# Optimization experiments

Measured on AMD Instinct MI355X. Metric: run time of the kernel, lower is better.

The kernel has to match this reference:

```python
import jax, jax.numpy as jnp
import numpy as np

B, T, C, H, D, E, K = 4, 1024, 1024, 16, 64, 8, 2
HID = 2 * D  # expert MLP hidden width (assumed 2*head_dim)
NEG = jnp.finfo(jnp.float32).min


def setup_inputs() -> dict:
    key = jax.random.key(0)
    ks = jax.random.split(key, 16)
    s = 0.02
    # rotary tables [max_pos, head_dim]
    inv_freq = 1.0 / (10000.0 ** (jnp.arange(0, D, 2, dtype=jnp.float32) / D))
    freqs = jnp.arange(T, dtype=jnp.float32)[:, None] * inv_freq[None, :]
    emb = jnp.concatenate([freqs, freqs], axis=-1)  # [T, D]
    return {
        "x": jax.random.normal(ks[0], (B, T, C), jnp.float32),
        "position_ids": jnp.sort(jax.random.randint(ks[1], (B, T), 0, T), axis=-1),
        "cos": jnp.cos(emb),
        "sin": jnp.sin(emb),
        "rq": s * jax.random.normal(ks[2], (D, E), jnp.float32),
        "rk": s * jax.random.normal(ks[3], (D, E), jnp.float32),
        "rv": s * jax.random.normal(ks[4], (D, E), jnp.float32),
        "q_w1": s * jax.random.normal(ks[5], (E, D, HID), jnp.float32),
        "q_w2": s * jax.random.normal(ks[6], (E, HID, D), jnp.float32),
        "k_w1": s * jax.random.normal(ks[7], (E, D, HID), jnp.float32),
        "k_w2": s * jax.random.normal(ks[8], (E, HID, D), jnp.float32),
        "v_w1": s * jax.random.normal(ks[9], (E, D, HID), jnp.float32),
        "v_w2": s * jax.random.normal(ks[10], (E, HID, D), jnp.float32),
        "o_w": s * jax.random.normal(ks[11], (C, C), jnp.float32),  # torch Linear weight [out,in]
    }


def _rotate_half(x):
    x1, x2 = x[..., : D // 2], x[..., D // 2:]
    return jnp.concatenate([-x2, x1], axis=-1)


def _moe_head_proj(xh, r_w, w1, w2):
    """Per-head top-k routed expert MLP. xh: [B,T,H,D]."""
    logits = jnp.einsum('bthd,de->bthe', xh, r_w)            # router logits
    vals, idx = jax.lax.top_k(logits, K)                     # [B,T,H,K]
    w = jax.nn.softmax(vals, axis=-1)
    onehot = jax.nn.one_hot(idx, E, dtype=xh.dtype)          # [B,T,H,K,E]
    w_full = jnp.einsum('bthk,bthke->bthe', w, onehot)       # scatter weights to all experts
    h = jax.nn.gelu(jnp.einsum('bthd,edf->bthef', xh, w1))   # all-expert hidden
    out = jnp.einsum('bthe,bthef,efg->bthg', w_full, h, w2)  # masked weighted combine
    return out, logits


def reference(x, position_ids, cos, sin, rq, rk, rv, q_w1, q_w2, k_w1, k_w2, v_w1, v_w2, o_w):
    xh = x.reshape(B, T, H, D)
    q, _ = _moe_head_proj(xh, rq, q_w1, q_w2)
    k, _ = _moe_head_proj(xh, rk, k_w1, k_w2)
    v, _ = _moe_head_proj(xh, rv, v_w1, v_w2)
    q = q.transpose(0, 2, 1, 3)  # [B,H,T,D]
    k = k.transpose(0, 2, 1, 3)
    v = v.transpose(0, 2, 1, 3)
    # RoPE
    c = cos[position_ids][:, None, :, :]  # [B,1,T,D]
    s = sin[position_ids][:, None, :, :]
    q = q * c + _rotate_half(q) * s
    k = k * c + _rotate_half(k) * s
    # causal SDPA
    scores = jnp.einsum('bhqd,bhkd->bhqk', q, k) / jnp.sqrt(jnp.float32(D))
    causal = jnp.tril(jnp.ones((T, T), dtype=bool))
    scores = jnp.where(causal, scores, NEG)
    attn = jax.nn.softmax(scores, axis=-1)
    out = jnp.einsum('bhqk,bhkd->bhqd', attn, v)
    out = out.transpose(0, 2, 1, 3).reshape(B, T, C)
    return out @ o_w.T
```

## Files before the change

### kernel.cpp

```cpp
#include <hip/hip_runtime.h>
#include <math.h>

#define BB 4
#define TT 1024
#define CCH 1024
#define HH 16
#define DD 64
#define EE 8
#define HID 128
#define CAP 8192
#define GEXP 504

typedef unsigned short u16;
typedef unsigned int u32;
typedef short bf16x8 __attribute__((ext_vector_type(8)));
typedef float f32x4 __attribute__((ext_vector_type(4)));

__device__ __forceinline__ u16 f2bf(float f) {
    unsigned int u = __float_as_uint(f);
    unsigned int r = (u + 0x7FFFu + ((u >> 16) & 1u)) >> 16;
    return (u16)r;
}
__device__ __forceinline__ u16 f2bf_f(float f) {
    return (u16)((__float_as_uint(f) + 0x8000u) >> 16);
}
__device__ __forceinline__ u32 pkbf(float lo, float hi) {
    u32 a = __float_as_uint(lo) + 0x8000u;
    u32 b = __float_as_uint(hi) + 0x8000u;
    return __builtin_amdgcn_perm(b, a, 0x07060302u);
}
__device__ __forceinline__ float gelu_fast(float z) {
    float t = z * z;
    float wn = __builtin_fmaf(t, -0.07135481283f, -1.5957691216f);
    float e = __expf(z * wn);
    return __fdividef(z, 1.f + e);
}

#define GLD16(gp, lp) __builtin_amdgcn_global_load_lds( \
    (const __attribute__((address_space(1))) u32*)(gp), \
    (__attribute__((address_space(3))) u32*)(lp), 16, 0, 0)

__global__ __launch_bounds__(256) void router_kernel(
    const float* __restrict__ x,
    const float* __restrict__ rq, const float* __restrict__ rk, const float* __restrict__ rv,
    unsigned int* __restrict__ counts,
    unsigned int* __restrict__ idxbuf, float2* __restrict__ wtbuf)
{
    const int tid = threadIdx.x;
    const unsigned int g = blockIdx.x * 256 + tid;

    __shared__ float rS[3][64][8];
    __shared__ int lcnt[192];
    __shared__ int lbase[192];

    for (int i = tid; i < 1536; i += 256) {
        int p = i >> 9, rem = i & 511;
        const float* rp = (p == 0) ? rq : (p == 1) ? rk : rv;
        rS[p][rem >> 3][rem & 7] = rp[rem];
    }
    if (tid < 192) lcnt[tid] = 0;
    __syncthreads();

    float lg[3][8];
    #pragma unroll
    for (int p = 0; p < 3; ++p)
        #pragma unroll
        for (int e = 0; e < 8; ++e) lg[p][e] = 0.f;

    const float* xr = x + (size_t)g * 64;
    for (int i4 = 0; i4 < 16; ++i4) {
        float4 xv = ((const float4*)xr)[i4];
        float xa[4] = {xv.x, xv.y, xv.z, xv.w};
        #pragma unroll
        for (int m = 0; m < 4; ++m) {
            int d = i4 * 4 + m;
            #pragma unroll
            for (int p = 0; p < 3; ++p) {
                float4 r0 = *(const float4*)&rS[p][d][0];
                float4 r1 = *(const float4*)&rS[p][d][4];
                lg[p][0] += xa[m] * r0.x; lg[p][1] += xa[m] * r0.y;
                lg[p][2] += xa[m] * r0.z; lg[p][3] += xa[m] * r0.w;
                lg[p][4] += xa[m] * r1.x; lg[p][5] += xa[m] * r1.y;
                lg[p][6] += xa[m] * r1.z; lg[p][7] += xa[m] * r1.w;
            }
        }
    }

    int ppe[3]; float2 pw[3]; int slot[3];
    #pragma unroll
    for (int p = 0; p < 3; ++p) {
        int i1 = 0; float v1 = lg[p][0];
        #pragma unroll
        for (int e = 1; e < 8; ++e) { if (lg[p][e] > v1) { v1 = lg[p][e]; i1 = e; } }
        int i2 = -1; float v2 = -3.402823466e38f;
        #pragma unroll
        for (int e = 0; e < 8; ++e) { if (e != i1 && lg[p][e] > v2) { v2 = lg[p][e]; i2 = e; } }
        float z = __expf(v2 - v1);
        float inv = 1.f / (1.f + z);
        float wa = inv, wb = z * inv;
        int lo = min(i1, i2), hi = max(i1, i2);
        float wlo = (i1 < i2) ? wa : wb;
        float whi = (i1 < i2) ? wb : wa;
        int pel = p * 64 + lo * 8 + hi;
        ppe[p] = pel; pw[p] = make_float2(wlo, whi);
        slot[p] = atomicAdd(&lcnt[pel], 1);
    }
    __syncthreads();
    if (tid < 192) {
        int c = lcnt[tid];
        lbase[tid] = c ? (int)atomicAdd(&counts[tid], (unsigned int)c) : 0;
    }
    __syncthreads();
    #pragma unroll
    for (int p = 0; p < 3; ++p) {
        int pos = lbase[ppe[p]] + slot[p];
        if (pos < CAP) {
            idxbuf[ppe[p] * CAP + pos] = g;
            wtbuf[ppe[p] * CAP + pos]  = pw[p];
        }
    }
}

__global__ __launch_bounds__(128) void sched_kernel(
    const unsigned int* __restrict__ counts, unsigned int* __restrict__ blockinfo)
{
    const int tid = threadIdx.x;
    __shared__ int nsub[84];
    __shared__ int extra[84];
    __shared__ int frac[84];
    __shared__ int alloc[84];
    __shared__ int startS[84];
    __shared__ int nnzS, totalS, rem2S;

    if (tid < 84) {
        int p = tid / 28, q = tid - 28 * p, lo = 0;
        while (q >= 7 - lo) { q -= 7 - lo; ++lo; }
        int hi = lo + 1 + q;
        int n = (int)counts[p * 64 + lo * 8 + hi];
        if (n > CAP) n = CAP;
        nsub[tid] = (n + 31) >> 5;
    }
    __syncthreads();
    if (tid == 0) {
        int tot = 0, nz = 0;
        for (int i = 0; i < 84; ++i) { tot += nsub[i]; nz += (nsub[i] > 0); }
        totalS = tot; nnzS = nz;
    }
    __syncthreads();
    const int R = GEXP - nnzS;
    if (tid < 84) {
        if (nsub[tid] > 0) {
            int e = (int)(((long long)nsub[tid] * R) / totalS);
            extra[tid] = e;
            frac[tid] = nsub[tid] * R - e * totalS;
        } else { extra[tid] = 0; frac[tid] = -1; }
    }
    __syncthreads();
    if (tid == 0) {
        int se = 0;
        for (int i = 0; i < 84; ++i) se += extra[i];
        rem2S = GEXP - nnzS - se;
    }
    __syncthreads();
    if (tid < 84) {
        if (nsub[tid] > 0) {
            int rank = 0;
            for (int j = 0; j < 84; ++j)
                if (nsub[j] > 0 && (frac[j] > frac[tid] || (frac[j] == frac[tid] && j < tid))) ++rank;
            alloc[tid] = 1 + extra[tid] + (rank < rem2S ? 1 : 0);
        } else alloc[tid] = 0;
    }
    __syncthreads();
    if (tid == 0) {
        int s = 0;
        for (int i = 0; i < 84; ++i) { startS[i] = s; s += alloc[i]; }
    }
    __syncthreads();
    if (tid < 84) {
        int a = alloc[tid], st = startS[tid];
        for (int c = 0; c < a; ++c)
            blockinfo[st + c] = (unsigned)tid | ((unsigned)c << 8) | ((unsigned)a << 20);
    }
}

__global__ __launch_bounds__(256) void wcvt_kernel(
    const float* __restrict__ qw1, const float* __restrict__ kw1, const float* __restrict__ vw1,
    const float* __restrict__ qw2, const float* __restrict__ kw2, const float* __restrict__ vw2,
    u16* __restrict__ img1, u16* __restrict__ img2)
{
    int t = blockIdx.x * 256 + threadIdx.x;
    u16 tmp[8];
    if (t < 24576) {
        int c = t & 7, f = (t >> 3) & 127, e = (t >> 10) & 7, p = t >> 13;
        const float* w1 = ((p == 0) ? qw1 : (p == 1) ? kw1 : vw1) + e * 8192;
        int dbase = 8 * (c ^ (f & 7));
        #pragma unroll
        for (int j = 0; j < 8; ++j) tmp[j] = f2bf(w1[(dbase + j) * 128 + f]);
        uint4 ov;
        ov.x = (u32)tmp[0] | ((u32)tmp[1] << 16);
        ov.y = (u32)tmp[2] | ((u32)tmp[3] << 16);
        ov.z = (u32)tmp[4] | ((u32)tmp[5] << 16);
        ov.w = (u32)tmp[6] | ((u32)tmp[7] << 16);
        ((uint4*)img1)[t] = ov;
    } else {
        int i = t - 24576;
        int c = i & 15, g = (i >> 4) & 63, e = (i >> 10) & 7, p = i >> 13;
        const float* w2 = ((p == 0) ? qw2 : (p == 1) ? kw2 : vw2) + e * 8192;
        int fbase = 8 * (c ^ (g & 15));
        #pragma unroll
        for (int j = 0; j < 8; ++j) tmp[j] = f2bf(w2[(fbase + j) * 64 + g]);
        uint4 ov;
        ov.x = (u32)tmp[0] | ((u32)tmp[1] << 16);
        ov.y = (u32)tmp[2] | ((u32)tmp[3] << 16);
        ov.z = (u32)tmp[4] | ((u32)tmp[5] << 16);
        ov.w = (u32)tmp[6] | ((u32)tmp[7] << 16);
        ((uint4*)img2)[i] = ov;
    }
}

__global__ __launch_bounds__(512, 2) void expert_kernel(
    const float* __restrict__ x, const int* __restrict__ pos_ids,
    const float* __restrict__ cosb, const float* __restrict__ sinb,
    const u16* __restrict__ img1, const u16* __restrict__ img2,
    const unsigned int* __restrict__ counts,
    const unsigned int* __restrict__ idxbuf, const float2* __restrict__ wtbuf,
    const unsigned int* __restrict__ blockinfo,
    u16* __restrict__ qb, u16* __restrict__ kb, u16* __restrict__ vb)
{
    const int tid = threadIdx.x;
    const unsigned int info = blockinfo[blockIdx.x];
    const int pe84 = info & 255;
    const int chunk = (info >> 8) & 0xFFF;
    const int nch = info >> 20;
    const int p = pe84 / 28;
    int q28 = pe84 - p * 28;
    int lo = 0;
    while (q28 >= 7 - lo) { q28 -= 7 - lo; ++lo; }
    const int hi = lo + 1 + q28;
    const int pe = p * 64 + lo * 8 + hi;

    int n = (int)counts[pe]; if (n == 0) return; if (n > CAP) n = CAP;

    u16* outp = (p == 0) ? qb : (p == 1) ? kb : vb;
    const unsigned int* il = idxbuf + pe * CAP;
    const float2* wl = wtbuf + pe * CAP;

    __shared__ __align__(16) u16 wsh[32768];

    {
        const u16* a0 = img1 + (p * 8 + lo) * 8192;
        const u16* b0 = img2 + (p * 8 + lo) * 8192;
        const u16* a1 = img1 + (p * 8 + hi) * 8192;
        const u16* b1 = img2 + (p * 8 + hi) * 8192;
        #pragma unroll
        for (int k = 0; k < 2; ++k) {
            int o = (k * 512 + tid) * 8;
            GLD16(a0 + o, wsh + o);
            GLD16(b0 + o, wsh + 8192 + o);
            GLD16(a1 + o, wsh + 16384 + o);
            GLD16(b1 + o, wsh + 24576 + o);
        }
    }
    __syncthreads();

    const int lane = tid & 63, w = tid >> 6, quad = lane >> 4, m16 = lane & 15;
    const int f7 = m16 & 7;
    const int sA = m16 + ((quad & 1) << 5);
    const int sB = sA + 16;
    const int wid = chunk * 8 + w;
    const int WRK = nch * 8;
    const int nsub = (n + 31) >> 5;

    for (int s = wid; s < nsub; s += WRK) {
        const int base = s * 32;
        unsigned int gtok = 0, obase = 0; float wlo_ = 0.f, whi_ = 0.f;
        int posv = 0, valid = 0;
        if (lane < 32) {
            int j = base + lane;
            valid = (j < n);
            int jc = valid ? j : (n - 1);
            gtok = il[jc];
            float2 wv = wl[jc];
            wlo_ = valid ? wv.x : 0.f; whi_ = valid ? wv.y : 0.f;
            unsigned int b_ = gtok >> 14, h_ = gtok & 15, t_ = (gtok >> 4) & 1023;
            obase = ((b_ * 16 + h_) * 1024 + t_) * 64;
            posv = pos_ids[b_ * 1024 + t_];
        }

        float wf00 = __shfl(wlo_, m16, 64);
        float wf10 = __shfl(whi_, m16, 64);
        float wf01 = __shfl(wlo_, 16 + m16, 64);
        float wf11 = __shfl(whi_, 16 + m16, 64);

        bf16x8 Afr[2][2];
        #pragma unroll
        for (int mt2 = 0; mt2 < 2; ++mt2) {
            unsigned int gm = (unsigned int)__shfl((int)gtok, mt2 * 16 + m16, 64);
            const float* xr = x + (size_t)gm * 64 + 8 * quad;
            float4 xa0 = *(const float4*)(xr);
            float4 xa1 = *(const float4*)(xr + 4);
            float4 xb0 = *(const float4*)(xr + 32);
            float4 xb1 = *(const float4*)(xr + 36);
            bf16x8 A0, A1;
            A0[0] = (short)f2bf_f(xa0.x); A0[1] = (short)f2bf_f(xa0.y);
            A0[2] = (short)f2bf_f(xa0.z); A0[3] = (short)f2bf_f(xa0.w);
            A0[4] = (short)f2bf_f(xa1.x); A0[5] = (short)f2bf_f(xa1.y);
            A0[6] = (short)f2bf_f(xa1.z); A0[7] = (short)f2bf_f(xa1.w);
            A1[0] = (short)f2bf_f(xb0.x); A1[1] = (short)f2bf_f(xb0.y);
            A1[2] = (short)f2bf_f(xb0.z); A1[3] = (short)f2bf_f(xb0.w);
            A1[4] = (short)f2bf_f(xb1.x); A1[5] = (short)f2bf_f(xb1.y);
            A1[6] = (short)f2bf_f(xb1.z); A1[7] = (short)f2bf_f(xb1.w);
            Afr[mt2][0] = A0; Afr[mt2][1] = A1;
        }

        f32x4 acc2[2][4];
        #pragma unroll
        for (int mt2 = 0; mt2 < 2; ++mt2)
            #pragma unroll
            for (int nt = 0; nt < 4; ++nt) acc2[mt2][nt] = (f32x4){0.f, 0.f, 0.f, 0.f};

        #pragma unroll 1
        for (int ekk = 0; ekk < 8; ++ekk) {
            const int e = ekk >> 2;
            const int kk = ekk & 3;
            const u16* w1b = wsh + e * 16384;
            const u16* w2b = w1b + 8192;
            const float wt0 = e ? wf10 : wf00;
            const float wt1 = e ? wf11 : wf01;

            f32x4 c[2][2];
            #pragma unroll
            for (int ntl = 0; ntl < 2; ++ntl) {
                const int f = 16 * (2 * kk + ntl) + m16;
                const u16* w1f = w1b + f * 64;
                bf16x8 wa = *(const bf16x8*)(w1f + (((quad    ) ^ f7) << 3));
                bf16x8 wb = *(const bf16x8*)(w1f + (((quad + 4) ^ f7) << 3));
                #pragma unroll
                for (int mt2 = 0; mt2 < 2; ++mt2) {
                    f32x4 t = (f32x4){0.f, 0.f, 0.f, 0.f};
                    t = __builtin_amdgcn_mfma_f32_16x16x32_bf16(wa, Afr[mt2][0], t, 0, 0, 0);
                    c[ntl][mt2] = __builtin_amdgcn_mfma_f32_16x16x32_bf16(wb, Afr[mt2][1], t, 0, 0, 0);
                }
            }
            const int c2base = (((4 * kk + quad) ^ m16) << 3);
            #pragma unroll
            for (int mt2 = 0; mt2 < 2; ++mt2) {
                const float wt = mt2 ? wt1 : wt0;
                u32 pl0, ph0, pl1, ph1;
                {
                    float g0 = wt * gelu_fast(c[0][mt2][0]);
                    float g1 = wt * gelu_fast(c[0][mt2][1]);
                    float g2 = wt * gelu_fast(c[0][mt2][2]);
                    float g3 = wt * gelu_fast(c[0][mt2][3]);
                    pl0 = pkbf(g0, g1); ph0 = pkbf(g2, g3);
                    g0 = wt * gelu_fast(c[1][mt2][0]);
                    g1 = wt * gelu_fast(c[1][mt2][1]);
                    g2 = wt * gelu_fast(c[1][mt2][2]);
                    g3 = wt * gelu_fast(c[1][mt2][3]);
                    pl1 = pkbf(g0, g1); ph1 = pkbf(g2, g3);
                }
                u32 q0l = (u32)__shfl((int)pl0, sA, 64);
                u32 q1l = (u32)__shfl((int)pl1, sA, 64);
                u32 q0h = (u32)__shfl((int)ph0, sA, 64);
                u32 q1h = (u32)__shfl((int)ph1, sA, 64);
                u32 r0l = (u32)__shfl((int)pl0, sB, 64);
                u32 r1l = (u32)__shfl((int)pl1, sB, 64);
                u32 r0h = (u32)__shfl((int)ph0, sB, 64);
                u32 r1h = (u32)__shfl((int)ph1, sB, 64);
                const bool hisel = (quad & 2);
                union { u32 u[4]; bf16x8 v; } a2;
                a2.u[0] = hisel ? q1l : q0l;
                a2.u[1] = hisel ? q1h : q0h;
                a2.u[2] = hisel ? r1l : r0l;
                a2.u[3] = hisel ? r1h : r0h;
                #pragma unroll
                for (int nt2 = 0; nt2 < 4; ++nt2) {
                    const u16* w2f = w2b + (16 * nt2 + m16) * 128 + c2base;
                    bf16x8 b2 = *(const bf16x8*)w2f;
                    acc2[mt2][nt2] = __builtin_amdgcn_mfma_f32_16x16x32_bf16(a2.v, b2, acc2[mt2][nt2], 0, 0, 0);
                }
            }
        }

        #pragma unroll
        for (int mt2 = 0; mt2 < 2; ++mt2) {
            #pragma unroll
            for (int r = 0; r < 4; ++r) {
                int tk = mt2 * 16 + 4 * quad + r;
                int   pos_r = __shfl(posv, tk, 64);
                unsigned int ob = (unsigned int)__shfl((int)obase, tk, 64);
                int   val_r = __shfl(valid, tk, 64);
                if (p < 2) {
                    #pragma unroll
                    for (int ntp = 0; ntp < 2; ++ntp) {
                        int d = 16 * ntp + m16;
                        float v1 = acc2[mt2][ntp][r];
                        float v2 = acc2[mt2][ntp + 2][r];
                        float cd = cosb[pos_r * 64 + d];
                        float sd = sinb[pos_r * 64 + d];
                        if (val_r) {
                            outp[ob + d]      = f2bf(v1 * cd - v2 * sd);
                            outp[ob + d + 32] = f2bf(v2 * cd + v1 * sd);
                        }
                    }
                } else {
                    #pragma unroll
                    for (int nt = 0; nt < 4; ++nt) {
                        float v = acc2[mt2][nt][r];
                        if (val_r) outp[ob + 16 * nt + m16] = f2bf(v);
                    }
                }
            }
        }
    }
}

__global__ __launch_bounds__(256) void cvt_bf16_kernel(
    const float* __restrict__ in, u16* __restrict__ out, int n4)
{
    int i = blockIdx.x * 256 + threadIdx.x;
    if (i >= n4) return;
    float4 v = ((const float4*)in)[i];
    unsigned int lov = (unsigned int)f2bf(v.x) | ((unsigned int)f2bf(v.y) << 16);
    unsigned int hiv = (unsigned int)f2bf(v.z) | ((unsigned int)f2bf(v.w) << 16);
    ((uint2*)out)[i] = make_uint2(lov, hiv);
}

__global__ __launch_bounds__(256) void attn_kernel(
    const u16* __restrict__ qbp, const u16* __restrict__ kbp,
    const u16* __restrict__ vbp, u16* __restrict__ ao)
{
    const int tid = threadIdx.x;
    const int i8 = blockIdx.x & 7;
    const int plane_i = blockIdx.x >> 3;
    const int h = plane_i & 15, b = plane_i >> 4;
    const size_t plane = (size_t)plane_i * 1024 * 64;
    const u16* qp = qbp + plane;
    const u16* kp = kbp + plane;
    const u16* vp = vbp + plane;

    const int w = tid >> 6, lane = tid & 63, quad = lane >> 4, m16 = lane & 15;
    const int row = tid >> 2, seg = tid & 3;
    const int kjv = tid & 63, dgv = tid >> 6;

    __shared__ u16 Ks[64][72];
    __shared__ u16 Vt[64][72];
    __shared__ u16 Ps[4][16][72];

    #pragma unroll 1
    for (int half = 0; half < 2; ++half) {
        const int qt = half ? (15 - i8) : i8;
        const int q0 = qt * 64;

        const u16* qrow = &qp[(size_t)(q0 + 16 * w + m16) * 64 + 8 * quad];
        bf16x8 aq0 = *(const bf16x8*)(qrow);
        bf16x8 aq1 = *(const bf16x8*)(qrow + 32);

        uint4 kr0, kr1; ushort4 vr0, vr1, vr2, vr3;
        {
            const uint4* src = (const uint4*)&kp[(size_t)row * 64 + seg * 16];
            kr0 = src[0]; kr1 = src[1];
            const u16* vb2 = &vp[(size_t)kjv * 64 + dgv * 4];
            vr0 = *(const ushort4*)(vb2);
            vr1 = *(const ushort4*)(vb2 + 16);
            vr2 = *(const ushort4*)(vb2 + 32);
            vr3 = *(const ushort4*)(vb2 + 48);
        }

        float m_r[4], l_r[4];
        #pragma unroll
        for (int i = 0; i < 4; ++i) { m_r[i] = -1e30f; l_r[i] = 0.f; }
        f32x4 oacc[4];
        #pragma unroll
        for (int i = 0; i < 4; ++i) oacc[i] = (f32x4){0.f, 0.f, 0.f, 0.f};

        for (int kt = 0; kt <= qt; ++kt) {
            __syncthreads();
            {
                uint4* dst = (uint4*)&Ks[row][seg * 16];
                dst[0] = kr0; dst[1] = kr1;
                int d0 = dgv * 4;
                Vt[d0 + 0][kjv] = vr0.x; Vt[d0 + 1][kjv] = vr0.y;
                Vt[d0 + 2][kjv] = vr0.z; Vt[d0 + 3][kjv] = vr0.w;
                Vt[d0 + 16][kjv] = vr1.x; Vt[d0 + 17][kjv] = vr1.y;
                Vt[d0 + 18][kjv] = vr1.z; Vt[d0 + 19][kjv] = vr1.w;
                Vt[d0 + 32][kjv] = vr2.x; Vt[d0 + 33][kjv] = vr2.y;
                Vt[d0 + 34][kjv] = vr2.z; Vt[d0 + 35][kjv] = vr2.w;
                Vt[d0 + 48][kjv] = vr3.x; Vt[d0 + 49][kjv] = vr3.y;
                Vt[d0 + 50][kjv] = vr3.z; Vt[d0 + 51][kjv] = vr3.w;
            }
            __syncthreads();
            if (kt < qt) {
                const int k0n = (kt + 1) * 64;
                const uint4* src = (const uint4*)&kp[(size_t)(k0n + row) * 64 + seg * 16];
                kr0 = src[0]; kr1 = src[1];
                const u16* vb2 = &vp[(size_t)(k0n + kjv) * 64 + dgv * 4];
                vr0 = *(const ushort4*)(vb2);
                vr1 = *(const ushort4*)(vb2 + 16);
                vr2 = *(const ushort4*)(vb2 + 32);
                vr3 = *(const ushort4*)(vb2 + 48);
            }

            f32x4 sv[4];
            #pragma unroll
            for (int ct = 0; ct < 4; ++ct) {
                bf16x8 bk0 = *(const bf16x8*)&Ks[16 * ct + m16][8 * quad];
                bf16x8 bk1 = *(const bf16x8*)&Ks[16 * ct + m16][32 + 8 * quad];
                f32x4 acc = (f32x4){0.f, 0.f, 0.f, 0.f};
                acc = __builtin_amdgcn_mfma_f32_16x16x32_bf16(aq0, bk0, acc, 0, 0, 0);
                acc = __builtin_amdgcn_mfma_f32_16x16x32_bf16(aq1, bk1, acc, 0, 0, 0);
                sv[ct] = acc;
            }

            float s[4][4];
            const bool diag = (kt == qt);
            #pragma unroll
            for (int ct = 0; ct < 4; ++ct)
                #pragma unroll
                for (int reg = 0; reg < 4; ++reg) {
                    float v = sv[ct][reg] * 0.125f;
                    if (diag) {
                        int col = 16 * ct + m16;
                        int rw = 16 * w + 4 * quad + reg;
                        if (col > rw) v = -1e30f;
                    }
                    s[ct][reg] = v;
                }

            float nm[4], al[4];
            #pragma unroll
            for (int reg = 0; reg < 4; ++reg) {
                float rm = fmaxf(fmaxf(s[0][reg], s[1][reg]), fmaxf(s[2][reg], s[3][reg]));
                #pragma unroll
                for (int off = 1; off < 16; off <<= 1) rm = fmaxf(rm, __shfl_xor(rm, off, 16));
                float mn = fmaxf(m_r[reg], rm);
                nm[reg] = mn;
                al[reg] = __expf(m_r[reg] - mn);
            }
            #pragma unroll
            for (int reg = 0; reg < 4; ++reg) {
                float sum = 0.f;
                #pragma unroll
                for (int ct = 0; ct < 4; ++ct) {
                    float pv = __expf(s[ct][reg] - nm[reg]);
                    s[ct][reg] = pv;
                    sum += pv;
                }
                #pragma unroll
                for (int off = 1; off < 16; off <<= 1) sum += __shfl_xor(sum, off, 16);
                l_r[reg] = l_r[reg] * al[reg] + sum;
                m_r[reg] = nm[reg];
            }

            #pragma unroll
            for (int ct = 0; ct < 4; ++ct)
                #pragma unroll
                for (int reg = 0; reg < 4; ++reg)
                    Ps[w][4 * quad + reg][16 * ct + m16] = f2bf(s[ct][reg]);

            #pragma unroll
            for (int dt = 0; dt < 4; ++dt)
                #pragma unroll
                for (int reg = 0; reg < 4; ++reg) oacc[dt][reg] *= al[reg];

            bf16x8 ap0 = *(const bf16x8*)&Ps[w][m16][8 * quad];
            bf16x8 ap1 = *(const bf16x8*)&Ps[w][m16][32 + 8 * quad];
            #pragma unroll
            for (int dt = 0; dt < 4; ++dt) {
                bf16x8 bv0 = *(const bf16x8*)&Vt[16 * dt + m16][8 * quad];
                bf16x8 bv1 = *(const bf16x8*)&Vt[16 * dt + m16][32 + 8 * quad];
                oacc[dt] = __builtin_amdgcn_mfma_f32_16x16x32_bf16(ap0, bv0, oacc[dt], 0, 0, 0);
                oacc[dt] = __builtin_amdgcn_mfma_f32_16x16x32_bf16(ap1, bv1, oacc[dt], 0, 0, 0);
            }
        }

        #pragma unroll
        for (int reg = 0; reg < 4; ++reg) {
            float linv = 1.f / l_r[reg];
            int rw = q0 + 16 * w + 4 * quad + reg;
            size_t base = ((size_t)(b * 1024) + rw) * 1024 + h * 64;
            #pragma unroll
            for (int dt = 0; dt < 4; ++dt)
                ao[base + 16 * dt + m16] = f2bf(oacc[dt][reg] * linv);
        }
    }
}

__global__ __launch_bounds__(256) void oproj_kernel(
    const u16* __restrict__ A, const u16* __restrict__ Bw,
    float* __restrict__ out)
{
    const int tid = threadIdx.x;
    const int bn = blockIdx.x & 7;
    const int bm = blockIdx.x >> 3;
    const int m0 = bm * 128, n0 = bn * 128;
    const int w = tid >> 6, lane = tid & 63, quad = lane >> 4, m16 = lane & 15;
    const int wm = (w >> 1) * 64, wn = (w & 1) * 64;

    __shared__ u16 As[128][32];
    __shared__ u16 Bs[128][32];

    f32x4 acc[4][4];
    #pragma unroll
    for (int mt = 0; mt < 4; ++mt)
        #pragma unroll
        for (int nt = 0; nt < 4; ++nt) acc[mt][nt] = (f32x4){0.f, 0.f, 0.f, 0.f};

    for (int k0 = 0; k0 < 1024; k0 += 32) {
        __syncthreads();
        {
            int rw = tid >> 1, sg = (tid & 1) * 16;
            const uint4* srcA = (const uint4*)&A[(size_t)(m0 + rw) * 1024 + k0 + sg];
            uint4 a0 = srcA[0], a1 = srcA[1];
            uint4* dstA = (uint4*)&As[rw][sg];
            dstA[0] = a0; dstA[1] = a1;
            const uint4* srcB = (const uint4*)&Bw[(size_t)(n0 + rw) * 1024 + k0 + sg];
            uint4 b0 = srcB[0], b1 = srcB[1];
            uint4* dstB = (uint4*)&Bs[rw][sg];
            dstB[0] = b0; dstB[1] = b1;
        }
        __syncthreads();
        bf16x8 af[4], bf_[4];
        #pragma unroll
        for (int mt = 0; mt < 4; ++mt) af[mt] = *(const bf16x8*)&As[wm + 16 * mt + m16][8 * quad];
        #pragma unroll
        for (int nt = 0; nt < 4; ++nt) bf_[nt] = *(const bf16x8*)&Bs[wn + 16 * nt + m16][8 * quad];
        #pragma unroll
        for (int mt = 0; mt < 4; ++mt)
            #pragma unroll
            for (int nt = 0; nt < 4; ++nt)
                acc[mt][nt] = __builtin_amdgcn_mfma_f32_16x16x32_bf16(af[mt], bf_[nt], acc[mt][nt], 0, 0, 0);
    }
    #pragma unroll
    for (int mt = 0; mt < 4; ++mt)
        #pragma unroll
        for (int nt = 0; nt < 4; ++nt)
            #pragma unroll
            for (int reg = 0; reg < 4; ++reg)
                out[(size_t)(m0 + wm + 16 * mt + 4 * quad + reg) * 1024 + n0 + wn + 16 * nt + m16] =
                    acc[mt][nt][reg];
}

extern "C" void kernel_launch(void* const* d_in, const int* in_sizes, int n_in,
                              void* d_out, int out_size, void* d_ws, size_t ws_size,
                              hipStream_t stream) {
    (void)in_sizes; (void)n_in; (void)out_size; (void)ws_size;
    const float* x    = (const float*)d_in[0];
    const int*   pid  = (const int*)  d_in[1];
    const float* cosb = (const float*)d_in[2];
    const float* sinb = (const float*)d_in[3];
    const float* rq   = (const float*)d_in[4];
    const float* rk   = (const float*)d_in[5];
    const float* rv   = (const float*)d_in[6];
    const float* qw1  = (const float*)d_in[7];
    const float* qw2  = (const float*)d_in[8];
    const float* kw1  = (const float*)d_in[9];
    const float* kw2  = (const float*)d_in[10];
    const float* vw1  = (const float*)d_in[11];
    const float* vw2  = (const float*)d_in[12];
    const float* ow   = (const float*)d_in[13];
    float* out = (float*)d_out;

    const size_t MB = 1u << 20;
    char* wsb = (char*)d_ws;
    u16* qb   = (u16*)(wsb + 0 * MB);
    u16* kb   = (u16*)(wsb + 8 * MB);
    u16* vb   = (u16*)(wsb + 16 * MB);
    u16* aobf = (u16*)(wsb + 24 * MB);
    u16* owbf = (u16*)(wsb + 32 * MB);
    unsigned int* idxbuf = (unsigned int*)(wsb + 34 * MB);
    float2*       wtbuf  = (float2*)(wsb + 41 * MB);
    unsigned int* counts = (unsigned int*)(wsb + 54 * MB);
    unsigned int* blockinfo = (unsigned int*)(wsb + 54 * MB + 4096);
    u16* w1img = (u16*)(wsb + 56 * MB);
    u16* w2img = (u16*)(wsb + 57 * MB);

    hipMemsetAsync(counts, 0, 1024, stream);

    hipLaunchKernelGGL(wcvt_kernel, dim3(192), dim3(256), 0, stream,
                       qw1, kw1, vw1, qw2, kw2, vw2, w1img, w2img);
    hipLaunchKernelGGL(router_kernel, dim3(256), dim3(256), 0, stream,
                       x, rq, rk, rv, counts, idxbuf, wtbuf);
    hipLaunchKernelGGL(sched_kernel, dim3(1), dim3(128), 0, stream,
                       counts, blockinfo);
    hipLaunchKernelGGL(cvt_bf16_kernel, dim3(1024), dim3(256), 0, stream,
                       ow, owbf, 1024 * 1024 / 4);
    hipLaunchKernelGGL(expert_kernel, dim3(GEXP), dim3(512), 0, stream,
                       x, pid, cosb, sinb, w1img, w2img,
                       counts, idxbuf, wtbuf, blockinfo, qb, kb, vb);
    hipLaunchKernelGGL(attn_kernel, dim3(512), dim3(256), 0, stream,
                       qb, kb, vb, aobf);
    hipLaunchKernelGGL(oproj_kernel, dim3(256), dim3(256), 0, stream,
                       aobf, owbf, out);
}
```

Measured before the change: 247.6 us.

## Fuse weight conversion, router and o_w cast into one prep kernel; split attention tiles

After: 282.5 us. 1.14x slower.

```diff
diff --git a/kernel.cpp b/kernel.cpp
--- a/kernel.cpp
+++ b/kernel.cpp
@@ -40,83 +40,132 @@
     (const __attribute__((address_space(1))) u32*)(gp), \
     (__attribute__((address_space(3))) u32*)(lp), 16, 0, 0)
 
-__global__ __launch_bounds__(256) void router_kernel(
+__global__ __launch_bounds__(256) void prep_kernel(
     const float* __restrict__ x,
     const float* __restrict__ rq, const float* __restrict__ rk, const float* __restrict__ rv,
     unsigned int* __restrict__ counts,
-    unsigned int* __restrict__ idxbuf, float2* __restrict__ wtbuf)
+    unsigned int* __restrict__ idxbuf, float2* __restrict__ wtbuf,
+    const float* __restrict__ qw1, const float* __restrict__ kw1, const float* __restrict__ vw1,
+    const float* __restrict__ qw2, const float* __restrict__ kw2, const float* __restrict__ vw2,
+    u16* __restrict__ img1, u16* __restrict__ img2,
+    const float* __restrict__ ow, u16* __restrict__ owbf)
 {
+    const int bi = blockIdx.x;
     const int tid = threadIdx.x;
-    const unsigned int g = blockIdx.x * 256 + tid;
-
-    __shared__ float rS[3][64][8];
-    __shared__ int lcnt[192];
-    __shared__ int lbase[192];
-
-    for (int i = tid; i < 1536; i += 256) {
-        int p = i >> 9, rem = i & 511;
-        const float* rp = (p == 0) ? rq : (p == 1) ? rk : rv;
-        rS[p][rem >> 3][rem & 7] = rp[rem];
-    }
-    if (tid < 192) lcnt[tid] = 0;
-    __syncthreads();
-
-    float lg[3][8];
-    #pragma unroll
-    for (int p = 0; p < 3; ++p)
-        #pragma unroll
-        for (int e = 0; e < 8; ++e) lg[p][e] = 0.f;
-
-    const float* xr = x + (size_t)g * 64;
-    for (int i4 = 0; i4 < 16; ++i4) {
-        float4 xv = ((const float4*)xr)[i4];
-        float xa[4] = {xv.x, xv.y, xv.z, xv.w};
-        #pragma unroll
-        for (int m = 0; m < 4; ++m) {
-            int d = i4 * 4 + m;
-            #pragma unroll
-            for (int p = 0; p < 3; ++p) {
-                float4 r0 = *(const float4*)&rS[p][d][0];
-                float4 r1 = *(const float4*)&rS[p][d][4];
-                lg[p][0] += xa[m] * r0.x; lg[p][1] += xa[m] * r0.y;
-                lg[p][2] += xa[m] * r0.z; lg[p][3] += xa[m] * r0.w;
-                lg[p][4] += xa[m] * r1.x; lg[p][5] += xa[m] * r1.y;
-                lg[p][6] += xa[m] * r1.z; lg[p][7] += xa[m] * r1.w;
+
+    if (bi < 192) {
+        int t = bi * 256 + tid;
+        u16 tmp[8];
+        if (t < 24576) {
+            int c = t & 7, f = (t >> 3) & 127, e = (t >> 10) & 7, p = t >> 13;
+            const float* w1 = ((p == 0) ? qw1 : (p == 1) ? kw1 : vw1) + e * 8192;
+            int dbase = 8 * (c ^ (f & 7));
+            #pragma unroll
+            for (int j = 0; j < 8; ++j) tmp[j] = f2bf(w1[(dbase + j) * 128 + f]);
+            uint4 ov;
+            ov.x = (u32)tmp[0] | ((u32)tmp[1] << 16);
+            ov.y = (u32)tmp[2] | ((u32)tmp[3] << 16);
+            ov.z = (u32)tmp[4] | ((u32)tmp[5] << 16);
+            ov.w = (u32)tmp[6] | ((u32)tmp[7] << 16);
+            ((uint4*)img1)[t] = ov;
+        } else {
+            int i = t - 24576;
+            int c = i & 15, g = (i >> 4) & 63, e = (i >> 10) & 7, p = i >> 13;
+            const float* w2 = ((p == 0) ? qw2 : (p == 1) ? kw2 : vw2) + e * 8192;
+            int fbase = 8 * (c ^ (g & 15));
+            #pragma unroll
+            for (int j = 0; j < 8; ++j) tmp[j] = f2bf(w2[(fbase + j) * 64 + g]);
+            uint4 ov;
+            ov.x = (u32)tmp[0] | ((u32)tmp[1] << 16);
+            ov.y = (u32)tmp[2] | ((u32)tmp[3] << 16);
+            ov.z = (u32)tmp[4] | ((u32)tmp[5] << 16);
+            ov.w = (u32)tmp[6] | ((u32)tmp[7] << 16);
+            ((uint4*)img2)[i] = ov;
+        }
+        return;
+    }
+
+    if (bi < 1216) {
+        int i = (bi - 192) * 256 + tid;
+        float4 v = ((const float4*)ow)[i];
+        unsigned int lov = (unsigned int)f2bf(v.x) | ((unsigned int)f2bf(v.y) << 16);
+        unsigned int hiv = (unsigned int)f2bf(v.z) | ((unsigned int)f2bf(v.w) << 16);
+        ((uint2*)owbf)[i] = make_uint2(lov, hiv);
+        return;
+    }
+
+    {
+        const unsigned int g = (bi - 1216) * 256 + tid;
+
+        __shared__ float rS[3][64][8];
+        __shared__ int lcnt[192];
+        __shared__ int lbase[192];
+
+        for (int i = tid; i < 1536; i += 256) {
+            int p = i >> 9, rem = i & 511;
+            const float* rp = (p == 0) ? rq : (p == 1) ? rk : rv;
+            rS[p][rem >> 3][rem & 7] = rp[rem];
+        }
+        if (tid < 192) lcnt[tid] = 0;
+        __syncthreads();
+
+        float lg[3][8];
+        #pragma unroll
+        for (int p = 0; p < 3; ++p)
+            #pragma unroll
+            for (int e = 0; e < 8; ++e) lg[p][e] = 0.f;
+
+        const float* xr = x + (size_t)g * 64;
+        for (int i4 = 0; i4 < 16; ++i4) {
+            float4 xv = ((const float4*)xr)[i4];
+            float xa[4] = {xv.x, xv.y, xv.z, xv.w};
+            #pragma unroll
+            for (int m = 0; m < 4; ++m) {
+                int d = i4 * 4 + m;
+                #pragma unroll
+                for (int p = 0; p < 3; ++p) {
+                    float4 r0 = *(const float4*)&rS[p][d][0];
+                    float4 r1 = *(const float4*)&rS[p][d][4];
+                    lg[p][0] += xa[m] * r0.x; lg[p][1] += xa[m] * r0.y;
+                    lg[p][2] += xa[m] * r0.z; lg[p][3] += xa[m] * r0.w;
+                    lg[p][4] += xa[m] * r1.x; lg[p][5] += xa[m] * r1.y;
+                    lg[p][6] += xa[m] * r1.z; lg[p][7] += xa[m] * r1.w;
+                }
             }
         }
-    }
-
-    int ppe[3]; float2 pw[3]; int slot[3];
-    #pragma unroll
-    for (int p = 0; p < 3; ++p) {
-        int i1 = 0; float v1 = lg[p][0];
-        #pragma unroll
-        for (int e = 1; e < 8; ++e) { if (lg[p][e] > v1) { v1 = lg[p][e]; i1 = e; } }
-        int i2 = -1; float v2 = -3.402823466e38f;
-        #pragma unroll
-        for (int e = 0; e < 8; ++e) { if (e != i1 && lg[p][e] > v2) { v2 = lg[p][e]; i2 = e; } }
-        float z = __expf(v2 - v1);
-        float inv = 1.f / (1.f + z);
-        float wa = inv, wb = z * inv;
-        int lo = min(i1, i2), hi = max(i1, i2);
-        float wlo = (i1 < i2) ? wa : wb;
-        float whi = (i1 < i2) ? wb : wa;
-        int pel = p * 64 + lo * 8 + hi;
-        ppe[p] = pel; pw[p] = make_float2(wlo, whi);
-        slot[p] = atomicAdd(&lcnt[pel], 1);
-    }
-    __syncthreads();
-    if (tid < 192) {
-        int c = lcnt[tid];
-        lbase[tid] = c ? (int)atomicAdd(&counts[tid], (unsigned int)c) : 0;
-    }
-    __syncthreads();
-    #pragma unroll
-    for (int p = 0; p < 3; ++p) {
-        int pos = lbase[ppe[p]] + slot[p];
-        if (pos < CAP) {
-            idxbuf[ppe[p] * CAP + pos] = g;
-            wtbuf[ppe[p] * CAP + pos]  = pw[p];
+
+        int ppe[3]; float2 pw[3]; int slot[3];
+        #pragma unroll
+        for (int p = 0; p < 3; ++p) {
+            int i1 = 0; float v1 = lg[p][0];
+            #pragma unroll
+            for (int e = 1; e < 8; ++e) { if (lg[p][e] > v1) { v1 = lg[p][e]; i1 = e; } }
+            int i2 = -1; float v2 = -3.402823466e38f;
+            #pragma unroll
+            for (int e = 0; e < 8; ++e) { if (e != i1 && lg[p][e] > v2) { v2 = lg[p][e]; i2 = e; } }
+            float z = __expf(v2 - v1);
+            float inv = 1.f / (1.f + z);
+            float wa = inv, wb = z * inv;
+            int lo = min(i1, i2), hi = max(i1, i2);
+            float wlo = (i1 < i2) ? wa : wb;
+            float whi = (i1 < i2) ? wb : wa;
+            int pel = p * 64 + lo * 8 + hi;
+            ppe[p] = pel; pw[p] = make_float2(wlo, whi);
+            slot[p] = atomicAdd(&lcnt[pel], 1);
+        }
+        __syncthreads();
+        if (tid < 192) {
+            int c = lcnt[tid];
+            lbase[tid] = c ? (int)atomicAdd(&counts[tid], (unsigned int)c) : 0;
+        }
+        __syncthreads();
+        #pragma unroll
+        for (int p = 0; p < 3; ++p) {
+            int pos = lbase[ppe[p]] + slot[p];
+            if (pos < CAP) {
+                idxbuf[ppe[p] * CAP + pos] = g;
+                wtbuf[ppe[p] * CAP + pos]  = pw[p];
+            }
         }
     }
 }
@@ -180,41 +229,6 @@
         int a = alloc[tid], st = startS[tid];
         for (int c = 0; c < a; ++c)
             blockinfo[st + c] = (unsigned)tid | ((unsigned)c << 8) | ((unsigned)a << 20);
-    }
-}
-
-__global__ __launch_bounds__(256) void wcvt_kernel(
-    const float* __restrict__ qw1, const float* __restrict__ kw1, const float* __restrict__ vw1,
-    const float* __restrict__ qw2, const float* __restrict__ kw2, const float* __restrict__ vw2,
-    u16* __restrict__ img1, u16* __restrict__ img2)
-{
-    int t = blockIdx.x * 256 + threadIdx.x;
-    u16 tmp[8];
-    if (t < 24576) {
-        int c = t & 7, f = (t >> 3) & 127, e = (t >> 10) & 7, p = t >> 13;
-        const float* w1 = ((p == 0) ? qw1 : (p == 1) ? kw1 : vw1) + e * 8192;
-        int dbase = 8 * (c ^ (f & 7));
-        #pragma unroll
-        for (int j = 0; j < 8; ++j) tmp[j] = f2bf(w1[(dbase + j) * 128 + f]);
-        uint4 ov;
-        ov.x = (u32)tmp[0] | ((u32)tmp[1] << 16);
-        ov.y = (u32)tmp[2] | ((u32)tmp[3] << 16);
-        ov.z = (u32)tmp[4] | ((u32)tmp[5] << 16);
-        ov.w = (u32)tmp[6] | ((u32)tmp[7] << 16);
-        ((uint4*)img1)[t] = ov;
-    } else {
-        int i = t - 24576;
-        int c = i & 15, g = (i >> 4) & 63, e = (i >> 10) & 7, p = i >> 13;
-        const float* w2 = ((p == 0) ? qw2 : (p == 1) ? kw2 : vw2) + e * 8192;
-        int fbase = 8 * (c ^ (g & 15));
-        #pragma unroll
-        for (int j = 0; j < 8; ++j) tmp[j] = f2bf(w2[(fbase + j) * 64 + g]);
-        uint4 ov;
-        ov.x = (u32)tmp[0] | ((u32)tmp[1] << 16);
-        ov.y = (u32)tmp[2] | ((u32)tmp[3] << 16);
-        ov.z = (u32)tmp[4] | ((u32)tmp[5] << 16);
-        ov.w = (u32)tmp[6] | ((u32)tmp[7] << 16);
-        ((uint4*)img2)[i] = ov;
     }
 }
 
@@ -415,24 +429,13 @@
     }
 }
 
-__global__ __launch_bounds__(256) void cvt_bf16_kernel(
-    const float* __restrict__ in, u16* __restrict__ out, int n4)
-{
-    int i = blockIdx.x * 256 + threadIdx.x;
-    if (i >= n4) return;
-    float4 v = ((const float4*)in)[i];
-    unsigned int lov = (unsigned int)f2bf(v.x) | ((unsigned int)f2bf(v.y) << 16);
-    unsigned int hiv = (unsigned int)f2bf(v.z) | ((unsigned int)f2bf(v.w) << 16);
-    ((uint2*)out)[i] = make_uint2(lov, hiv);
-}
-
 __global__ __launch_bounds__(256) void attn_kernel(
     const u16* __restrict__ qbp, const u16* __restrict__ kbp,
     const u16* __restrict__ vbp, u16* __restrict__ ao)
 {
     const int tid = threadIdx.x;
-    const int i8 = blockIdx.x & 7;
-    const int plane_i = blockIdx.x >> 3;
+    const int qt = 15 - (blockIdx.x & 15);
+    const int plane_i = blockIdx.x >> 4;
     const int h = plane_i & 15, b = plane_i >> 4;
     const size_t plane = (size_t)plane_i * 1024 * 64;
     const u16* qp = qbp + plane;
@@ -447,142 +450,138 @@
     __shared__ u16 Vt[64][72];
     __shared__ u16 Ps[4][16][72];
 
-    #pragma unroll 1
-    for (int half = 0; half < 2; ++half) {
-        const int qt = half ? (15 - i8) : i8;
-        const int q0 = qt * 64;
-
-        const u16* qrow = &qp[(size_t)(q0 + 16 * w + m16) * 64 + 8 * quad];
-        bf16x8 aq0 = *(const bf16x8*)(qrow);
-        bf16x8 aq1 = *(const bf16x8*)(qrow + 32);
-
-        uint4 kr0, kr1; ushort4 vr0, vr1, vr2, vr3;
+    const int q0 = qt * 64;
+
+    const u16* qrow = &qp[(size_t)(q0 + 16 * w + m16) * 64 + 8 * quad];
+    bf16x8 aq0 = *(const bf16x8*)(qrow);
+    bf16x8 aq1 = *(const bf16x8*)(qrow + 32);
+
+    uint4 kr0, kr1; ushort4 vr0, vr1, vr2, vr3;
+    {
+        const uint4* src = (const uint4*)&kp[(size_t)row * 64 + seg * 16];
+        kr0 = src[0]; kr1 = src[1];
+        const u16* vb2 = &vp[(size_t)kjv * 64 + dgv * 4];
+        vr0 = *(const ushort4*)(vb2);
+        vr1 = *(const ushort4*)(vb2 + 16);
+        vr2 = *(const ushort4*)(vb2 + 32);
+        vr3 = *(const ushort4*)(vb2 + 48);
+    }
+
+    float m_r[4], l_r[4];
+    #pragma unroll
+    for (int i = 0; i < 4; ++i) { m_r[i] = -1e30f; l_r[i] = 0.f; }
+    f32x4 oacc[4];
+    #pragma unroll
+    for (int i = 0; i < 4; ++i) oacc[i] = (f32x4){0.f, 0.f, 0.f, 0.f};
+
+    for (int kt = 0; kt <= qt; ++kt) {
+        __syncthreads();
         {
-            const uint4* src = (const uint4*)&kp[(size_t)row * 64 + seg * 16];
+            uint4* dst = (uint4*)&Ks[row][seg * 16];
+            dst[0] = kr0; dst[1] = kr1;
+            int d0 = dgv * 4;
+            Vt[d0 + 0][kjv] = vr0.x; Vt[d0 + 1][kjv] = vr0.y;
+            Vt[d0 + 2][kjv] = vr0.z; Vt[d0 + 3][kjv] = vr0.w;
+            Vt[d0 + 16][kjv] = vr1.x; Vt[d0 + 17][kjv] = vr1.y;
+            Vt[d0 + 18][kjv] = vr1.z; Vt[d0 + 19][kjv] = vr1.w;
+            Vt[d0 + 32][kjv] = vr2.x; Vt[d0 + 33][kjv] = vr2.y;
+            Vt[d0 + 34][kjv] = vr2.z; Vt[d0 + 35][kjv] = vr2.w;
+            Vt[d0 + 48][kjv] = vr3.x; Vt[d0 + 49][kjv] = vr3.y;
+            Vt[d0 + 50][kjv] = vr3.z; Vt[d0 + 51][kjv] = vr3.w;
+        }
+        __syncthreads();
+        if (kt < qt) {
+            const int k0n = (kt + 1) * 64;
+            const uint4* src = (const uint4*)&kp[(size_t)(k0n + row) * 64 + seg * 16];
             kr0 = src[0]; kr1 = src[1];
-            const u16* vb2 = &vp[(size_t)kjv * 64 + dgv * 4];
+            const u16* vb2 = &vp[(size_t)(k0n + kjv) * 64 + dgv * 4];
             vr0 = *(const ushort4*)(vb2);
             vr1 = *(const ushort4*)(vb2 + 16);
             vr2 = *(const ushort4*)(vb2 + 32);
             vr3 = *(const ushort4*)(vb2 + 48);
         }
 
-        float m_r[4], l_r[4];
-        #pragma unroll
-        for (int i = 0; i < 4; ++i) { m_r[i] = -1e30f; l_r[i] = 0.f; }
-        f32x4 oacc[4];
-        #pragma unroll
-        for (int i = 0; i < 4; ++i) oacc[i] = (f32x4){0.f, 0.f, 0.f, 0.f};
-
-        for (int kt = 0; kt <= qt; ++kt) {
-            __syncthreads();
-            {
-                uint4* dst = (uint4*)&Ks[row][seg * 16];
-                dst[0] = kr0; dst[1] = kr1;
-                int d0 = dgv * 4;
-                Vt[d0 + 0][kjv] = vr0.x; Vt[d0 + 1][kjv] = vr0.y;
-                Vt[d0 + 2][kjv] = vr0.z; Vt[d0 + 3][kjv] = vr0.w;
-                Vt[d0 + 16][kjv] = vr1.x; Vt[d0 + 17][kjv] = vr1.y;
-                Vt[d0 + 18][kjv] = vr1.z; Vt[d0 + 19][kjv] = vr1.w;
-                Vt[d0 + 32][kjv] = vr2.x; Vt[d0 + 33][kjv] = vr2.y;
-                Vt[d0 + 34][kjv] = vr2.z; Vt[d0 + 35][kjv] = vr2.w;
-                Vt[d0 + 48][kjv] = vr3.x; Vt[d0 + 49][kjv] = vr3.y;
-                Vt[d0 + 50][kjv] = vr3.z; Vt[d0 + 51][kjv] = vr3.w;
+        f32x4 sv[4];
+        #pragma unroll
+        for (int ct = 0; ct < 4; ++ct) {
+            bf16x8 bk0 = *(const bf16x8*)&Ks[16 * ct + m16][8 * quad];
+            bf16x8 bk1 = *(const bf16x8*)&Ks[16 * ct + m16][32 + 8 * quad];
+            f32x4 acc = (f32x4){0.f, 0.f, 0.f, 0.f};
+            acc = __builtin_amdgcn_mfma_f32_16x16x32_bf16(aq0, bk0, acc, 0, 0, 0);
+            acc = __builtin_amdgcn_mfma_f32_16x16x32_bf16(aq1, bk1, acc, 0, 0, 0);
+            sv[ct] = acc;
+        }
+
+        float s[4][4];
+        const bool diag = (kt == qt);
+        #pragma unroll
+        for (int ct = 0; ct < 4; ++ct)
+            #pragma unroll
+            for (int reg = 0; reg < 4; ++reg) {
+                float v = sv[ct][reg] * 0.125f;
+                if (diag) {
+                    int col = 16 * ct + m16;
+                    int rw = 16 * w + 4 * quad + reg;
+                    if (col > rw) v = -1e30f;
+                }
+                s[ct][reg] = v;
             }
-            __syncthreads();
-            if (kt < qt) {
-                const int k0n = (kt + 1) * 64;
-                const uint4* src = (const uint4*)&kp[(size_t)(k0n + row) * 64 + seg * 16];
-                kr0 = src[0]; kr1 = src[1];
-                const u16* vb2 = &vp[(size_t)(k0n + kjv) * 64 + dgv * 4];
-                vr0 = *(const ushort4*)(vb2);
-                vr1 = *(const ushort4*)(vb2 + 16);
-                vr2 = *(const ushort4*)(vb2 + 32);
-                vr3 = *(const ushort4*)(vb2 + 48);
+
+        float nm[4], al[4];
+        #pragma unroll
+        for (int reg = 0; reg < 4; ++reg) {
+            float rm = fmaxf(fmaxf(s[0][reg], s[1][reg]), fmaxf(s[2][reg], s[3][reg]));
+            #pragma unroll
+            for (int off = 1; off < 16; off <<= 1) rm = fmaxf(rm, __shfl_xor(rm, off, 16));
+            float mn = fmaxf(m_r[reg], rm);
+            nm[reg] = mn;
+            al[reg] = __expf(m_r[reg] - mn);
+        }
+        #pragma unroll
+        for (int reg = 0; reg < 4; ++reg) {
+            float sum = 0.f;
+            #pragma unroll
+            for (int ct = 0; ct < 4; ++ct) {
+                float pv = __expf(s[ct][reg] - nm[reg]);
+                s[ct][reg] = pv;
+                sum += pv;
             }
-
-            f32x4 sv[4];
-            #pragma unroll
-            for (int ct = 0; ct < 4; ++ct) {
-                bf16x8 bk0 = *(const bf16x8*)&Ks[16 * ct + m16][8 * quad];
-                bf16x8 bk1 = *(const bf16x8*)&Ks[16 * ct + m16][32 + 8 * quad];
-                f32x4 acc = (f32x4){0.f, 0.f, 0.f, 0.f};
-                acc = __builtin_amdgcn_mfma_f32_16x16x32_bf16(aq0, bk0, acc, 0, 0, 0);
-                acc = __builtin_amdgcn_mfma_f32_16x16x32_bf16(aq1, bk1, acc, 0, 0, 0);
-                sv[ct] = acc;
-            }
-
-            float s[4][4];
-            const bool diag = (kt == qt);
-            #pragma unroll
-            for (int ct = 0; ct < 4; ++ct)
-                #pragma unroll
-                for (int reg = 0; reg < 4; ++reg) {
-                    float v = sv[ct][reg] * 0.125f;
-                    if (diag) {
-                        int col = 16 * ct + m16;
-                        int rw = 16 * w + 4 * quad + reg;
-                        if (col > rw) v = -1e30f;
-                    }
-                    s[ct][reg] = v;
-                }
-
-            float nm[4], al[4];
-            #pragma unroll
-            for (int reg = 0; reg < 4; ++reg) {
-                float rm = fmaxf(fmaxf(s[0][reg], s[1][reg]), fmaxf(s[2][reg], s[3][reg]));
-                #pragma unroll
-                for (int off = 1; off < 16; off <<= 1) rm = fmaxf(rm, __shfl_xor(rm, off, 16));
-                float mn = fmaxf(m_r[reg], rm);
-                nm[reg] = mn;
-                al[reg] = __expf(m_r[reg] - mn);
-            }
-            #pragma unroll
-            for (int reg = 0; reg < 4; ++reg) {
-                float sum = 0.f;
-                #pragma unroll
-                for (int ct = 0; ct < 4; ++ct) {
-                    float pv = __expf(s[ct][reg] - nm[reg]);
-                    s[ct][reg] = pv;
-                    sum += pv;
-                }
-                #pragma unroll
-                for (int off = 1; off < 16; off <<= 1) sum += __shfl_xor(sum, off, 16);
-                l_r[reg] = l_r[reg] * al[reg] + sum;
-                m_r[reg] = nm[reg];
-            }
-
-            #pragma unroll
-            for (int ct = 0; ct < 4; ++ct)
-                #pragma unroll
-                for (int reg = 0; reg < 4; ++reg)
-                    Ps[w][4 * quad + reg][16 * ct + m16] = f2bf(s[ct][reg]);
-
-            #pragma unroll
-            for (int dt = 0; dt < 4; ++dt)
-                #pragma unroll
-                for (int reg = 0; reg < 4; ++reg) oacc[dt][reg] *= al[reg];
-
-            bf16x8 ap0 = *(const bf16x8*)&Ps[w][m16][8 * quad];
-            bf16x8 ap1 = *(const bf16x8*)&Ps[w][m16][32 + 8 * quad];
-            #pragma unroll
-            for (int dt = 0; dt < 4; ++dt) {
-                bf16x8 bv0 = *(const bf16x8*)&Vt[16 * dt + m16][8 * quad];
-                bf16x8 bv1 = *(const bf16x8*)&Vt[16 * dt + m16][32 + 8 * quad];
-                oacc[dt] = __builtin_amdgcn_mfma_f32_16x16x32_bf16(ap0, bv0, oacc[dt], 0, 0, 0);
-                oacc[dt] = __builtin_amdgcn_mfma_f32_16x16x32_bf16(ap1, bv1, oacc[dt], 0, 0, 0);
-            }
-        }
-
-        #pragma unroll
-        for (int reg = 0; reg < 4; ++reg) {
-            float linv = 1.f / l_r[reg];
-            int rw = q0 + 16 * w + 4 * quad + reg;
-            size_t base = ((size_t)(b * 1024) + rw) * 1024 + h * 64;
-            #pragma unroll
-            for (int dt = 0; dt < 4; ++dt)
-                ao[base + 16 * dt + m16] = f2bf(oacc[dt][reg] * linv);
-        }
+            #pragma unroll
+            for (int off = 1; off < 16; off <<= 1) sum += __shfl_xor(sum, off, 16);
+            l_r[reg] = l_r[reg] * al[reg] + sum;
+            m_r[reg] = nm[reg];
+        }
+
+        #pragma unroll
+        for (int ct = 0; ct < 4; ++ct)
+            #pragma unroll
+            for (int reg = 0; reg < 4; ++reg)
+                Ps[w][4 * quad + reg][16 * ct + m16] = f2bf(s[ct][reg]);
+
+        #pragma unroll
+        for (int dt = 0; dt < 4; ++dt)
+            #pragma unroll
+            for (int reg = 0; reg < 4; ++reg) oacc[dt][reg] *= al[reg];
+
+        bf16x8 ap0 = *(const bf16x8*)&Ps[w][m16][8 * quad];
+        bf16x8 ap1 = *(const bf16x8*)&Ps[w][m16][32 + 8 * quad];
+        #pragma unroll
+        for (int dt = 0; dt < 4; ++dt) {
+            bf16x8 bv0 = *(const bf16x8*)&Vt[16 * dt + m16][8 * quad];
+            bf16x8 bv1 = *(const bf16x8*)&Vt[16 * dt + m16][32 + 8 * quad];
+            oacc[dt] = __builtin_amdgcn_mfma_f32_16x16x32_bf16(ap0, bv0, oacc[dt], 0, 0, 0);
+            oacc[dt] = __builtin_amdgcn_mfma_f32_16x16x32_bf16(ap1, bv1, oacc[dt], 0, 0, 0);
+        }
+    }
+
+    #pragma unroll
+    for (int reg = 0; reg < 4; ++reg) {
+        float linv = 1.f / l_r[reg];
+        int rw = q0 + 16 * w + 4 * quad + reg;
+        size_t base = ((size_t)(b * 1024) + rw) * 1024 + h * 64;
+        #pragma unroll
+        for (int dt = 0; dt < 4; ++dt)
+            ao[base + 16 * dt + m16] = f2bf(oacc[dt][reg] * linv);
     }
 }
 
@@ -677,18 +676,16 @@
 
     hipMemsetAsync(counts, 0, 1024, stream);
 
-    hipLaunchKernelGGL(wcvt_kernel, dim3(192), dim3(256), 0, stream,
-                       qw1, kw1, vw1, qw2, kw2, vw2, w1img, w2img);
-    hipLaunchKernelGGL(router_kernel, dim3(256), dim3(256), 0, stream,
-                       x, rq, rk, rv, counts, idxbuf, wtbuf);
+    hipLaunchKernelGGL(prep_kernel, dim3(1472), dim3(256), 0, stream,
+                       x, rq, rk, rv, counts, idxbuf, wtbuf,
+                       qw1, kw1, vw1, qw2, kw2, vw2, w1img, w2img,
+                       ow, owbf);
     hipLaunchKernelGGL(sched_kernel, dim3(1), dim3(128), 0, stream,
                        counts, blockinfo);
-    hipLaunchKernelGGL(cvt_bf16_kernel, dim3(1024), dim3(256), 0, stream,
-                       ow, owbf, 1024 * 1024 / 4);
     hipLaunchKernelGGL(expert_kernel, dim3(GEXP), dim3(512), 0, stream,
                        x, pid, cosb, sinb, w1img, w2img,
                        counts, idxbuf, wtbuf, blockinfo, qb, kb, vb);
-    hipLaunchKernelGGL(attn_kernel, dim3(512), dim3(256), 0, stream,
+    hipLaunchKernelGGL(attn_kernel, dim3(1024), dim3(256), 0, stream,
                        qb, kb, vb, aobf);
     hipLaunchKernelGGL(oproj_kernel, dim3(256), dim3(256), 0, stream,
                        aobf, owbf, out);
```
